# Performance work log

Hardware: AMD Instinct MI355X
Metric: run time of the kernel (lower is better)

Reference implementation:

```python
import jax, jax.numpy as jnp
import numpy as np

B, L_VLM, L_EXP = 4, 768, 64
L_TOT = L_VLM + L_EXP
D_VLM, D_EXP = 2048, 1024
H, DH = 8, 256
ROPE_BASE = 10000.0
SCALE = 1.0 / np.sqrt(DH).astype(np.float32)


def setup_inputs() -> dict:
    key = jax.random.key(0)
    ks = jax.random.split(key, 12)
    s = 0.02  # weight init scale
    return {
        "vlm_hidden": jax.random.normal(ks[0], (B, L_VLM, D_VLM), jnp.float32),
        "exp_hidden": jax.random.normal(ks[1], (B, L_EXP, D_EXP), jnp.float32),
        "attention_mask": jnp.zeros((B, 1, L_TOT, L_TOT), jnp.float32),  # additive mask
        "position_ids": jnp.broadcast_to(jnp.arange(L_TOT, dtype=jnp.int32)[None, :], (B, L_TOT)),
        "wq_v": jax.random.normal(ks[2], (D_VLM, H * DH), jnp.float32) * s,
        "wk_v": jax.random.normal(ks[3], (D_VLM, H * DH), jnp.float32) * s,
        "wv_v": jax.random.normal(ks[4], (D_VLM, H * DH), jnp.float32) * s,
        "wo_v": jax.random.normal(ks[5], (H * DH, D_VLM), jnp.float32) * s,
        "wq_e": jax.random.normal(ks[6], (D_EXP, H * DH), jnp.float32) * s,
        "wk_e": jax.random.normal(ks[7], (D_EXP, H * DH), jnp.float32) * s,
        "wv_e": jax.random.normal(ks[8], (D_EXP, H * DH), jnp.float32) * s,
        "wo_e": jax.random.normal(ks[9], (H * DH, D_EXP), jnp.float32) * s,
    }


def _proj(hs, w):
    # [B, L, D] @ [D, H*DH] -> [B, H, L, DH]
    b, l, _ = hs.shape
    return jnp.einsum('bld,de->ble', hs, w).reshape(b, l, H, DH).transpose(0, 2, 1, 3)


def _rope(x, cos, sin):
    # NeoX-style rotate-half (Gemma / vLLM RotaryEmbedding with rotary_dim == head_dim)
    d2 = x.shape[-1] // 2
    x1, x2 = x[..., :d2], x[..., d2:]
    return jnp.concatenate([x1 * cos - x2 * sin, x2 * cos + x1 * sin], axis=-1)


def reference(vlm_hidden, exp_hidden, attention_mask, position_ids,
              wq_v, wk_v, wv_v, wo_v, wq_e, wk_e, wv_e, wo_e):
    # 1) separate per-stream Q/K/V projections, 2) concat along sequence dim
    q = jnp.concatenate([_proj(vlm_hidden, wq_v), _proj(exp_hidden, wq_e)], axis=2)
    k = jnp.concatenate([_proj(vlm_hidden, wk_v), _proj(exp_hidden, wk_e)], axis=2)
    v = jnp.concatenate([_proj(vlm_hidden, wv_v), _proj(exp_hidden, wv_e)], axis=2)

    # 3) rotary positional embedding on the joint sequence
    inv_freq = 1.0 / (ROPE_BASE ** (jnp.arange(0, DH, 2, dtype=jnp.float32) / DH))  # [DH/2]
    freqs = position_ids.astype(jnp.float32)[:, :, None] * inv_freq                 # [B, L, DH/2]
    cos = jnp.cos(freqs)[:, None]  # [B, 1, L, DH/2]
    sin = jnp.sin(freqs)[:, None]
    q = _rope(q, cos, sin)
    k = _rope(k, cos, sin)

    # 4) masked attention over the joint sequence
    scores = jnp.einsum('bhqd,bhkd->bhqk', q, k) * SCALE + attention_mask
    probs = jax.nn.softmax(scores, axis=-1)
    out = jnp.einsum('bhqk,bhkd->bhqd', probs, v)              # [B, H, L, DH]
    out = out.transpose(0, 2, 1, 3).reshape(B, L_TOT, H * DH)  # [B, L, H*DH]

    # 5) split back and apply per-stream output projections
    vlm_out = jnp.einsum('ble,ed->bld', out[:, :L_VLM], wo_v)
    exp_out = jnp.einsum('ble,ed->bld', out[:, L_VLM:], wo_e)
    return vlm_out, exp_out
```

## Files before the change

### kernel.cpp

```cpp
#include <hip/hip_runtime.h>

typedef unsigned short u16;
using bf16x8 = __attribute__((ext_vector_type(8))) __bf16;
using f32x4  = __attribute__((ext_vector_type(4))) float;

__device__ __forceinline__ u16 f2bf(float f) {
  unsigned u = __builtin_bit_cast(unsigned, f);
  u += 0x7FFFu + ((u >> 16) & 1u);
  return (u16)(u >> 16);
}
__device__ __forceinline__ float bf2f(u16 s) {
  unsigned u = ((unsigned)s) << 16;
  return __builtin_bit_cast(float, u);
}
__device__ __forceinline__ void lds16(const void* g, void* l) {
  __builtin_amdgcn_global_load_lds(
      (const __attribute__((address_space(1))) void*)g,
      (__attribute__((address_space(3))) void*)l, 16, 0, 0);
}

__device__ __forceinline__ void gemm128(
    const u16* a0, const u16* a1, const u16* b0, const u16* b1,
    int ksteps, int t, u16* As, u16* Bs, f32x4 acc[4][4])
{
  const int lane = t & 63;
  u16* dA0 = As + t * 8;
  u16* dA1 = As + t * 8 + 2048;
  u16* dB0 = Bs + t * 8;
  u16* dB1 = Bs + t * 8 + 2048;

  const int wm = t >> 7;
  const int wn = (t >> 6) & 1;
  const int swz = (((lane >> 4) ^ (lane & 3)) * 8);
  const int fa = (wm * 64 + (lane & 15)) * 32 + swz;
  const int fb = (wn * 64 + (lane & 15)) * 32 + swz;

  for (int ks = 0; ks < ksteps; ++ks) {
    lds16(a0, dA0);
    lds16(a1, dA1);
    lds16(b0, dB0);
    lds16(b1, dB1);
    a0 += 32; a1 += 32; b0 += 32; b1 += 32;
    __syncthreads();
    bf16x8 af[4], bfr[4];
#pragma unroll
    for (int i = 0; i < 4; ++i) af[i]  = *(const bf16x8*)(As + fa + i * 512);
#pragma unroll
    for (int i = 0; i < 4; ++i) bfr[i] = *(const bf16x8*)(Bs + fb + i * 512);
#pragma unroll
    for (int mt = 0; mt < 4; ++mt)
#pragma unroll
      for (int nt = 0; nt < 4; ++nt)
        acc[mt][nt] = __builtin_amdgcn_mfma_f32_16x16x32_bf16(
            af[mt], bfr[nt], acc[mt][nt], 0, 0, 0);
    __syncthreads();
  }
}

struct PrepArgs {
  const float* tsrc[8]; u16* tdst[8]; int tK[8]; int tN[8];
  const float* csrc[2]; u16* cdst[2]; int cn4[2];
};

__global__ __launch_bounds__(256) void g_prep(PrepArgs a)
{
  __shared__ float T[32][33];
  const int z = blockIdx.z;
  if (z < 8) {
    const int Krows = a.tK[z], Ncols = a.tN[z];
    const int k0 = blockIdx.y * 32, n0 = blockIdx.x * 32;
    if (k0 >= Krows || n0 >= Ncols) return;
    const float* W = a.tsrc[z];
    u16* Wt = a.tdst[z];
    const int tx = threadIdx.x & 31, ty = threadIdx.x >> 5;
#pragma unroll
    for (int r = 0; r < 4; ++r)
      T[ty + r * 8][tx] = W[(size_t)(k0 + ty + r * 8) * Ncols + n0 + tx];
    __syncthreads();
#pragma unroll
    for (int r = 0; r < 4; ++r)
      Wt[(size_t)(n0 + ty + r * 8) * Krows + k0 + tx] = f2bf(T[tx][ty + r * 8]);
  } else {
    const int j = z - 8;
    const int n4 = a.cn4[j];
    const float* X = a.csrc[j];
    u16* Y = a.cdst[j];
    const int blk = blockIdx.y * gridDim.x + blockIdx.x;
    const int stride = gridDim.x * gridDim.y * 256;
    for (int i = blk * 256 + threadIdx.x; i < n4; i += stride) {
      float4 f = ((const float4*)X)[i];
      ushort4 u;
      u.x = f2bf(f.x); u.y = f2bf(f.y); u.z = f2bf(f.z); u.w = f2bf(f.w);
      ((ushort4*)Y)[i] = u;
    }
  }
}

__global__ __launch_bounds__(256) void g_proj_qkv(
    const u16* __restrict__ Xv, const u16* __restrict__ Xe,
    const u16* __restrict__ Wv_cat, const u16* __restrict__ We_cat,
    u16* __restrict__ Qb, u16* __restrict__ Kb, u16* __restrict__ Vt)
{
  __shared__ u16 As[4096], Bs[4096];
  const int z = blockIdx.z;
  const u16* X; const u16* Wt; int Kdim, rows_pb, l_off;
  if (z == 0) { X = Xv; Wt = Wv_cat; Kdim = 2048; rows_pb = 768; l_off = 0; }
  else {
    if (blockIdx.y >= 2) return;
    X = Xe; Wt = We_cat; Kdim = 1024; rows_pb = 64; l_off = 768;
  }
  const int t = threadIdx.x;
  const int m0 = blockIdx.y * 128, n0 = blockIdx.x * 128;
  const int r0 = t >> 2;
  const int cs = ((t & 3) ^ (r0 & 3)) * 8;
  const u16* a0 = X + (size_t)(m0 + r0) * Kdim + cs;
  const u16* a1 = X + (size_t)(m0 + r0 + 64) * Kdim + cs;
  const u16* b0 = Wt + (size_t)(n0 + r0) * Kdim + cs;
  const u16* b1 = Wt + (size_t)(n0 + r0 + 64) * Kdim + cs;

  f32x4 acc[4][4] = {};
  gemm128(a0, a1, b0, b1, Kdim >> 5, t, As, Bs, acc);

  const int lane = t & 63;
  const int rbase = m0 + (t >> 7) * 64 + ((lane >> 4) << 2);
  const int cbase = n0 + ((t >> 6) & 1) * 64 + (lane & 15);
  const int sect = n0 >> 11;

  if (sect < 2) {
    u16* Out = (sect == 0) ? Qb : Kb;
#pragma unroll
    for (int mt = 0; mt < 4; ++mt) {
#pragma unroll
      for (int r = 0; r < 4; ++r) {
        int m = rbase + mt * 16 + r;
        int b = m / rows_pb;
        int l = m - b * rows_pb + l_off;
#pragma unroll
        for (int nt = 0; nt < 4; ++nt) {
          int nloc = (cbase + nt * 16) & 2047;
          Out[(((size_t)(b * 8 + (nloc >> 8))) * 832 + l) * 256 + (nloc & 255)] =
              f2bf(acc[mt][nt][r]);
        }
      }
    }
  } else {
#pragma unroll
    for (int mt = 0; mt < 4; ++mt) {
      int mb = rbase + mt * 16;
      int b = mb / rows_pb;
      int l = mb - b * rows_pb + l_off;
#pragma unroll
      for (int nt = 0; nt < 4; ++nt) {
        int nloc = (cbase + nt * 16) & 2047;
        ushort4 p;
        p.x = f2bf(acc[mt][nt][0]); p.y = f2bf(acc[mt][nt][1]);
        p.z = f2bf(acc[mt][nt][2]); p.w = f2bf(acc[mt][nt][3]);
        *(ushort4*)&Vt[(((size_t)(b * 8 + (nloc >> 8))) * 256 + (nloc & 255)) * 832 + l] = p;
      }
    }
  }
}

__global__ __launch_bounds__(128) void g_rope(
    u16* __restrict__ Q, u16* __restrict__ Kx, const int* __restrict__ pos)
{
  const int blk = blockIdx.x;
  const int l = blk % 832, bh = blk / 832, b = bh >> 3;
  const int i = threadIdx.x;
  const float p = (float)pos[b * 832 + l];
  const float inv = exp2f(-(float)i * 0.103810252965229910f);
  const float ang = p * inv;
  const float c = cosf(ang), s = sinf(ang);
  const size_t base = ((size_t)bh * 832 + l) * 256;

  float x1 = bf2f(Q[base + i]), x2 = bf2f(Q[base + i + 128]);
  Q[base + i]       = f2bf((x1 * c - x2 * s) * 0.0625f);
  Q[base + i + 128] = f2bf((x2 * c + x1 * s) * 0.0625f);
  x1 = bf2f(Kx[base + i]); x2 = bf2f(Kx[base + i + 128]);
  Kx[base + i]       = f2bf(x1 * c - x2 * s);
  Kx[base + i + 128] = f2bf(x2 * c + x1 * s);
}

__global__ __launch_bounds__(256) void g_flash(
    const u16* __restrict__ Qb, const u16* __restrict__ Kb,
    const u16* __restrict__ Vt, const float* __restrict__ mask,
    u16* __restrict__ AO)
{
  __shared__ __align__(16) u16 Ks[8192];
  __shared__ __align__(16) u16 Vs[8192];
  __shared__ __align__(16) u16 Ps[2048];
  const int t = threadIdx.x;
  const int lane = t & 63, w = t >> 6, quad = lane >> 4;
  const int wb = w * 512;

  const int id = blockIdx.x;
  const int x = id & 7, k = id >> 3;
  const int bh = x + 8 * (k / 13);
  const int q0 = (k % 13) * 64;
  const int b = bh >> 3, h = bh & 7;

  const u16* Ksrc = Kb + (size_t)bh * 832 * 256;
  const u16* Vsrc = Vt + (size_t)bh * 256 * 832;
  const float* Mrow = mask + (size_t)b * 832 * 832;

  bf16x8 qf[8];
#pragma unroll
  for (int kf = 0; kf < 8; ++kf)
    qf[kf] = *(const bf16x8*)(
        Qb + ((size_t)bh * 832 + q0 + w * 16 + (lane & 15)) * 256 +
        kf * 32 + quad * 8);

  float mrun[4], lrun[4];
#pragma unroll
  for (int r = 0; r < 4; ++r) { mrun[r] = -3e38f; lrun[r] = 0.f; }
  f32x4 oa[16] = {};

  for (int kt = 0; kt < 26; ++kt) {
    __syncthreads();
#pragma unroll
    for (int p = 0; p < 4; ++p) {
      int c = p * 256 + t;
      int row = c >> 5, chk = c & 31;
      lds16(Ksrc + (size_t)(kt * 32 + row) * 256 + ((chk ^ (row & 7)) * 8),
            Ks + c * 8);
    }
#pragma unroll
    for (int p = 0; p < 4; ++p) {
      int c = p * 256 + t;
      int row = c >> 3;
      int lc = (c & 7) ^ (row & 7);
      int dh = 2 * row + (lc >> 2);
      lds16(Vsrc + (size_t)dh * 832 + kt * 32 + (lc & 3) * 8, Vs + c * 8);
    }
    __syncthreads();

    f32x4 sa[2] = {};
#pragma unroll
    for (int ks = 0; ks < 8; ++ks)
#pragma unroll
      for (int nt = 0; nt < 2; ++nt) {
        int krow = nt * 16 + (lane & 15);
        bf16x8 kb = *(const bf16x8*)(
            Ks + krow * 256 + (((ks * 4 + quad) ^ (krow & 7)) * 8));
        sa[nt] = __builtin_amdgcn_mfma_f32_16x16x32_bf16(qf[ks], kb, sa[nt], 0, 0, 0);
      }

    float alpha[4];
#pragma unroll
    for (int r = 0; r < 4; ++r) {
      int prow = quad * 4 + r;
      int q = q0 + w * 16 + prow;
      const float* mrp = Mrow + (size_t)q * 832 + kt * 32 + (lane & 15);
      float v0 = sa[0][r] + mrp[0];
      float v1 = sa[1][r] + mrp[16];
      float mx = fmaxf(v0, v1);
      mx = fmaxf(mx, __shfl_xor(mx, 1));
      mx = fmaxf(mx, __shfl_xor(mx, 2));
      mx = fmaxf(mx, __shfl_xor(mx, 4));
      mx = fmaxf(mx, __shfl_xor(mx, 8));
      float mn = fmaxf(mrun[r], mx);
      float al = __expf(mrun[r] - mn);
      float p0 = __expf(v0 - mn), p1 = __expf(v1 - mn);
      float rs = p0 + p1;
      rs += __shfl_xor(rs, 1);
      rs += __shfl_xor(rs, 2);
      rs += __shfl_xor(rs, 4);
      rs += __shfl_xor(rs, 8);
      lrun[r] = lrun[r] * al + rs;
      mrun[r] = mn;
      alpha[r] = al;
      int s0 = ((lane >> 3) & 1) ^ quad;
      int s1 = (2 | ((lane >> 3) & 1)) ^ quad;
      Ps[wb + prow * 32 + s0 * 8 + (lane & 7)] = f2bf(p0);
      Ps[wb + prow * 32 + s1 * 8 + (lane & 7)] = f2bf(p1);
    }

#pragma unroll
    for (int nt = 0; nt < 16; ++nt)
#pragma unroll
      for (int r = 0; r < 4; ++r) oa[nt][r] *= alpha[r];

    int prow2 = lane & 15;
    bf16x8 pa = *(const bf16x8*)(
        Ps + wb + prow2 * 32 + ((quad ^ ((prow2 >> 2) & 3)) * 8));
#pragma unroll
    for (int nt = 0; nt < 16; ++nt) {
      int dh = nt * 16 + (lane & 15);
      int row = dh >> 1;
      int lc = ((dh & 1) << 2) | quad;
      bf16x8 vb = *(const bf16x8*)(Vs + row * 64 + ((lc ^ (row & 7)) * 8));
      oa[nt] = __builtin_amdgcn_mfma_f32_16x16x32_bf16(pa, vb, oa[nt], 0, 0, 0);
    }
  }

  float linv[4];
#pragma unroll
  for (int r = 0; r < 4; ++r) linv[r] = 1.0f / lrun[r];
#pragma unroll
  for (int r = 0; r < 4; ++r) {
    size_t l = q0 + w * 16 + quad * 4 + r;
    u16* dst = AO + ((size_t)b * 832 + l) * 2048 + h * 256 + (lane & 15);
#pragma unroll
    for (int nt = 0; nt < 16; ++nt)
      dst[nt * 16] = f2bf(oa[nt][r] * linv[r]);
  }
}

__global__ __launch_bounds__(256) void g_oproj2(
    const u16* __restrict__ AO, const u16* __restrict__ Wov,
    const u16* __restrict__ Woe, float* __restrict__ out)
{
  __shared__ u16 As[4096], Bs[4096];
  const int z = blockIdx.z;
  const u16* Wt; float* C; int N, rows_pb, l_off;
  if (z == 0) { Wt = Wov; C = out; N = 2048; rows_pb = 768; l_off = 0; }
  else {
    if (blockIdx.y >= 2 || blockIdx.x >= 8) return;
    Wt = Woe; C = out + (size_t)4 * 768 * 2048; N = 1024; rows_pb = 64; l_off = 768;
  }
  const int t = threadIdx.x;
  const int m0 = blockIdx.y * 128, n0 = blockIdx.x * 128;
  const int r0 = t >> 2;
  const int cs = ((t & 3) ^ (r0 & 3)) * 8;
  int mr0 = m0 + r0, mr1 = m0 + r0 + 64;
  int ba = mr0 / rows_pb, bb = mr1 / rows_pb;
  const u16* a0 = AO + ((size_t)ba * 832 + (mr0 - ba * rows_pb) + l_off) * 2048 + cs;
  const u16* a1 = AO + ((size_t)bb * 832 + (mr1 - bb * rows_pb) + l_off) * 2048 + cs;
  const u16* b0 = Wt + (size_t)(n0 + r0) * 2048 + cs;
  const u16* b1 = Wt + (size_t)(n0 + r0 + 64) * 2048 + cs;

  f32x4 acc[4][4] = {};
  gemm128(a0, a1, b0, b1, 64, t, As, Bs, acc);

  const int lane = t & 63;
  const int rbase = m0 + (t >> 7) * 64 + ((lane >> 4) << 2);
  const int cbase = n0 + ((t >> 6) & 1) * 64 + (lane & 15);
#pragma unroll
  for (int mt = 0; mt < 4; ++mt)
#pragma unroll
    for (int r = 0; r < 4; ++r) {
      size_t m = rbase + mt * 16 + r;
#pragma unroll
      for (int nt = 0; nt < 4; ++nt)
        C[m * N + cbase + nt * 16] = acc[mt][nt][r];
    }
}

extern "C" void kernel_launch(void* const* d_in, const int* in_sizes, int n_in,
                              void* d_out, int out_size, void* d_ws, size_t ws_size,
                              hipStream_t stream)
{
  const float* vlm_h = (const float*)d_in[0];
  const float* exp_h = (const float*)d_in[1];
  const float* mask  = (const float*)d_in[2];
  const int*   pos   = (const int*)d_in[3];
  const float* wq_v  = (const float*)d_in[4];
  const float* wk_v  = (const float*)d_in[5];
  const float* wv_v  = (const float*)d_in[6];
  const float* wo_v  = (const float*)d_in[7];
  const float* wq_e  = (const float*)d_in[8];
  const float* wk_e  = (const float*)d_in[9];
  const float* wv_e  = (const float*)d_in[10];
  const float* wo_e  = (const float*)d_in[11];
  float* out = (float*)d_out;

  u16* U = (u16*)d_ws;
  u16* Xv   = U; U += (size_t)4 * 768 * 2048;
  u16* Xe   = U; U += (size_t)4 * 64 * 1024;
  u16* Wcv  = U; U += (size_t)6144 * 2048;
  u16* Wce  = U; U += (size_t)6144 * 1024;
  u16* Wov  = U; U += (size_t)2048 * 2048;
  u16* Woe  = U; U += (size_t)1024 * 2048;
  u16* Qb   = U; U += (size_t)32 * 832 * 256;
  u16* Kb   = U; U += (size_t)32 * 832 * 256;
  u16* Vt   = U; U += (size_t)32 * 256 * 832;
  u16* AO   = U; U += (size_t)4 * 832 * 2048;

  const dim3 blk(256);

  PrepArgs pa;
  pa.tsrc[0] = wq_v; pa.tdst[0] = Wcv;                        pa.tK[0] = 2048; pa.tN[0] = 2048;
  pa.tsrc[1] = wk_v; pa.tdst[1] = Wcv + (size_t)2048 * 2048;  pa.tK[1] = 2048; pa.tN[1] = 2048;
  pa.tsrc[2] = wv_v; pa.tdst[2] = Wcv + (size_t)4096 * 2048;  pa.tK[2] = 2048; pa.tN[2] = 2048;
  pa.tsrc[3] = wo_v; pa.tdst[3] = Wov;                        pa.tK[3] = 2048; pa.tN[3] = 2048;
  pa.tsrc[4] = wq_e; pa.tdst[4] = Wce;                        pa.tK[4] = 1024; pa.tN[4] = 2048;
  pa.tsrc[5] = wk_e; pa.tdst[5] = Wce + (size_t)2048 * 1024;  pa.tK[5] = 1024; pa.tN[5] = 2048;
  pa.tsrc[6] = wv_e; pa.tdst[6] = Wce + (size_t)4096 * 1024;  pa.tK[6] = 1024; pa.tN[6] = 2048;
  pa.tsrc[7] = wo_e; pa.tdst[7] = Woe;                        pa.tK[7] = 2048; pa.tN[7] = 1024;
  pa.csrc[0] = vlm_h; pa.cdst[0] = Xv; pa.cn4[0] = 1572864;
  pa.csrc[1] = exp_h; pa.cdst[1] = Xe; pa.cn4[1] = 65536;
  g_prep<<<dim3(64, 64, 10), blk, 0, stream>>>(pa);

  g_proj_qkv<<<dim3(48, 24, 2), blk, 0, stream>>>(Xv, Xe, Wcv, Wce, Qb, Kb, Vt);

  g_rope<<<dim3(32 * 832), dim3(128), 0, stream>>>(Qb, Kb, pos);

  g_flash<<<dim3(416), blk, 0, stream>>>(Qb, Kb, Vt, mask, AO);

  g_oproj2<<<dim3(16, 24, 2), blk, 0, stream>>>(AO, Wov, Woe, out);
}
```

Baseline: 456.3 us.

## Pipeline projection GEMMs with double-buffered LDS prefetch and phased MFMA scheduling

Replaces the single-stage GEMM core, which loaded one 32-wide K slice and synchronized twice per step, with a double-buffered 64-wide K pipeline. Global-to-LDS loads for upcoming tiles are issued in sub-phases, interleaved with MFMA groups, and paced with explicit vmcnt waits, barriers and setprio. The LDS swizzle changes to match the new fragment addressing. The goal is to hide global load latency behind matrix math in the QKV and output projections, at the cost of four times the LDS per block, which may lower occupancy, and fragile hand-tuned wait counts.

```diff
diff --git a/kernel.cpp b/kernel.cpp
--- a/kernel.cpp
+++ b/kernel.cpp
@@ -19,41 +19,110 @@
       (__attribute__((address_space(3))) void*)l, 16, 0, 0);
 }
 
-__device__ __forceinline__ void gemm128(
-    const u16* a0, const u16* a1, const u16* b0, const u16* b1,
-    int ksteps, int t, u16* As, u16* Bs, f32x4 acc[4][4])
+#define PH_SYNC() \
+  __builtin_amdgcn_s_barrier(); \
+  asm volatile("s_waitcnt lgkmcnt(0)" ::: "memory"); \
+  __builtin_amdgcn_sched_barrier(0);
+
+#define MFMA8(MA, MB) \
+  __builtin_amdgcn_s_setprio(1); \
+  acc[MA][0] = __builtin_amdgcn_mfma_f32_16x16x32_bf16(a0, b0, acc[MA][0], 0, 0, 0); \
+  acc[MB][0] = __builtin_amdgcn_mfma_f32_16x16x32_bf16(a1, b0, acc[MB][0], 0, 0, 0); \
+  acc[MA][1] = __builtin_amdgcn_mfma_f32_16x16x32_bf16(a0, b1, acc[MA][1], 0, 0, 0); \
+  acc[MB][1] = __builtin_amdgcn_mfma_f32_16x16x32_bf16(a1, b1, acc[MB][1], 0, 0, 0); \
+  acc[MA][2] = __builtin_amdgcn_mfma_f32_16x16x32_bf16(a0, b2, acc[MA][2], 0, 0, 0); \
+  acc[MB][2] = __builtin_amdgcn_mfma_f32_16x16x32_bf16(a1, b2, acc[MB][2], 0, 0, 0); \
+  acc[MA][3] = __builtin_amdgcn_mfma_f32_16x16x32_bf16(a0, b3, acc[MA][3], 0, 0, 0); \
+  acc[MB][3] = __builtin_amdgcn_mfma_f32_16x16x32_bf16(a1, b3, acc[MB][3], 0, 0, 0); \
+  __builtin_amdgcn_s_setprio(0);
+
+__device__ __forceinline__ void gemm_dp(
+    const u16* aR0, const u16* aR1, const u16* bR0, const u16* bR1,
+    int NT, int t, u16* As, u16* Bs, f32x4 acc[4][4])
 {
   const int lane = t & 63;
-  u16* dA0 = As + t * 8;
-  u16* dA1 = As + t * 8 + 2048;
-  u16* dB0 = Bs + t * 8;
-  u16* dB1 = Bs + t * 8 + 2048;
-
-  const int wm = t >> 7;
-  const int wn = (t >> 6) & 1;
-  const int swz = (((lane >> 4) ^ (lane & 3)) * 8);
-  const int fa = (wm * 64 + (lane & 15)) * 32 + swz;
-  const int fb = (wn * 64 + (lane & 15)) * 32 + swz;
-
-  for (int ks = 0; ks < ksteps; ++ks) {
-    lds16(a0, dA0);
-    lds16(a1, dA1);
-    lds16(b0, dB0);
-    lds16(b1, dB1);
-    a0 += 32; a1 += 32; b0 += 32; b1 += 32;
-    __syncthreads();
-    bf16x8 af[4], bfr[4];
-#pragma unroll
-    for (int i = 0; i < 4; ++i) af[i]  = *(const bf16x8*)(As + fa + i * 512);
-#pragma unroll
-    for (int i = 0; i < 4; ++i) bfr[i] = *(const bf16x8*)(Bs + fb + i * 512);
-#pragma unroll
-    for (int mt = 0; mt < 4; ++mt)
-#pragma unroll
-      for (int nt = 0; nt < 4; ++nt)
-        acc[mt][nt] = __builtin_amdgcn_mfma_f32_16x16x32_bf16(
-            af[mt], bfr[nt], acc[mt][nt], 0, 0, 0);
-    __syncthreads();
+  const int fr = lane & 15;
+  const int sA = ((lane >> 4) ^ ((fr >> 1) & 3)) << 3;
+  const int offA = (((t >> 7) & 1) * 64 + fr) * 32 + sA;
+  const int offB = (((t >> 6) & 1) * 64 + fr) * 32 + sA;
+
+  lds16(aR0,      As + t * 8);
+  lds16(aR1,      As + 2048 + t * 8);
+  lds16(bR0,      Bs + t * 8);
+  lds16(bR1,      Bs + 2048 + t * 8);
+  lds16(aR0 + 32, As + 4096 + t * 8);
+  lds16(aR1 + 32, As + 4096 + 2048 + t * 8);
+  lds16(bR0 + 32, Bs + 4096 + t * 8);
+  lds16(bR1 + 32, Bs + 4096 + 2048 + t * 8);
+  lds16(bR0 + 64, Bs + 8192 + t * 8);
+  lds16(bR1 + 64, Bs + 8192 + 2048 + t * 8);
+  lds16(aR0 + 64, As + 8192 + t * 8);
+  lds16(aR1 + 64, As + 8192 + 2048 + t * 8);
+  lds16(bR0 + 96, Bs + 8192 + 4096 + t * 8);
+  lds16(bR1 + 96, Bs + 8192 + 4096 + 2048 + t * 8);
+  asm volatile("s_waitcnt vmcnt(10)" ::: "memory");
+  __builtin_amdgcn_s_barrier();
+
+  for (int T = 0; T < NT; ++T) {
+    const int p = T & 1;
+    u16* Ab = As + p * 8192;
+    u16* Bb = Bs + p * 8192;
+    u16* An = As + (p ^ 1) * 8192;
+    const bool s1 = (T + 1 < NT), s2 = (T + 2 < NT);
+    const int k1 = (T + 1) * 64, k2 = (T + 2) * 64;
+    bf16x8 a0, a1, b0, b1, b2, b3;
+
+    a0 = *(const bf16x8*)(Ab + offA);
+    a1 = *(const bf16x8*)(Ab + offA + 512);
+    b0 = *(const bf16x8*)(Bb + offB);
+    b1 = *(const bf16x8*)(Bb + offB + 512);
+    b2 = *(const bf16x8*)(Bb + offB + 1024);
+    b3 = *(const bf16x8*)(Bb + offB + 1536);
+    if (s1) {
+      lds16(aR0 + k1 + 32, An + 4096 + t * 8);
+      lds16(aR1 + k1 + 32, An + 4096 + 2048 + t * 8);
+    }
+    PH_SYNC();
+    MFMA8(0, 1);
+    __builtin_amdgcn_s_barrier();
+
+    a0 = *(const bf16x8*)(Ab + offA + 1024);
+    a1 = *(const bf16x8*)(Ab + offA + 1536);
+    if (s2) {
+      lds16(bR0 + k2, Bb + t * 8);
+      lds16(bR1 + k2, Bb + 2048 + t * 8);
+    }
+    PH_SYNC();
+    MFMA8(2, 3);
+    if (s2) asm volatile("s_waitcnt vmcnt(10)" ::: "memory");
+    else    asm volatile("s_waitcnt vmcnt(0)"  ::: "memory");
+    __builtin_amdgcn_s_barrier();
+
+    a0 = *(const bf16x8*)(Ab + offA + 4096);
+    a1 = *(const bf16x8*)(Ab + offA + 4096 + 512);
+    b0 = *(const bf16x8*)(Bb + offB + 4096);
+    b1 = *(const bf16x8*)(Bb + offB + 4096 + 512);
+    b2 = *(const bf16x8*)(Bb + offB + 4096 + 1024);
+    b3 = *(const bf16x8*)(Bb + offB + 4096 + 1536);
+    if (s2) {
+      lds16(aR0 + k2, Ab + t * 8);
+      lds16(aR1 + k2, Ab + 2048 + t * 8);
+    }
+    PH_SYNC();
+    MFMA8(0, 1);
+    __builtin_amdgcn_s_barrier();
+
+    a0 = *(const bf16x8*)(Ab + offA + 4096 + 1024);
+    a1 = *(const bf16x8*)(Ab + offA + 4096 + 1536);
+    if (s2) {
+      lds16(bR0 + k2 + 32, Bb + 4096 + t * 8);
+      lds16(bR1 + k2 + 32, Bb + 4096 + 2048 + t * 8);
+    }
+    PH_SYNC();
+    MFMA8(2, 3);
+    if (s2) asm volatile("s_waitcnt vmcnt(10)" ::: "memory");
+    else    asm volatile("s_waitcnt vmcnt(0)"  ::: "memory");
+    __builtin_amdgcn_s_barrier();
   }
 }
 
@@ -101,7 +170,7 @@
     const u16* __restrict__ Wv_cat, const u16* __restrict__ We_cat,
     u16* __restrict__ Qb, u16* __restrict__ Kb, u16* __restrict__ Vt)
 {
-  __shared__ u16 As[4096], Bs[4096];
+  __shared__ __align__(16) u16 As[16384], Bs[16384];
   const int z = blockIdx.z;
   const u16* X; const u16* Wt; int Kdim, rows_pb, l_off;
   if (z == 0) { X = Xv; Wt = Wv_cat; Kdim = 2048; rows_pb = 768; l_off = 0; }
@@ -112,14 +181,14 @@
   const int t = threadIdx.x;
   const int m0 = blockIdx.y * 128, n0 = blockIdx.x * 128;
   const int r0 = t >> 2;
-  const int cs = ((t & 3) ^ (r0 & 3)) * 8;
-  const u16* a0 = X + (size_t)(m0 + r0) * Kdim + cs;
-  const u16* a1 = X + (size_t)(m0 + r0 + 64) * Kdim + cs;
-  const u16* b0 = Wt + (size_t)(n0 + r0) * Kdim + cs;
-  const u16* b1 = Wt + (size_t)(n0 + r0 + 64) * Kdim + cs;
+  const int sw = ((t & 3) ^ ((t >> 3) & 3)) * 8;
+  const u16* a0 = X + (size_t)(m0 + r0) * Kdim + sw;
+  const u16* a1 = X + (size_t)(m0 + r0 + 64) * Kdim + sw;
+  const u16* b0 = Wt + (size_t)(n0 + r0) * Kdim + sw;
+  const u16* b1 = Wt + (size_t)(n0 + r0 + 64) * Kdim + sw;
 
   f32x4 acc[4][4] = {};
-  gemm128(a0, a1, b0, b1, Kdim >> 5, t, As, Bs, acc);
+  gemm_dp(a0, a1, b0, b1, Kdim >> 6, t, As, Bs, acc);
 
   const int lane = t & 63;
   const int rbase = m0 + (t >> 7) * 64 + ((lane >> 4) << 2);
@@ -310,7 +379,7 @@
     const u16* __restrict__ AO, const u16* __restrict__ Wov,
     const u16* __restrict__ Woe, float* __restrict__ out)
 {
-  __shared__ u16 As[4096], Bs[4096];
+  __shared__ __align__(16) u16 As[16384], Bs[16384];
   const int z = blockIdx.z;
   const u16* Wt; float* C; int N, rows_pb, l_off;
   if (z == 0) { Wt = Wov; C = out; N = 2048; rows_pb = 768; l_off = 0; }
@@ -321,16 +390,16 @@
   const int t = threadIdx.x;
   const int m0 = blockIdx.y * 128, n0 = blockIdx.x * 128;
   const int r0 = t >> 2;
-  const int cs = ((t & 3) ^ (r0 & 3)) * 8;
+  const int sw = ((t & 3) ^ ((t >> 3) & 3)) * 8;
   int mr0 = m0 + r0, mr1 = m0 + r0 + 64;
   int ba = mr0 / rows_pb, bb = mr1 / rows_pb;
-  const u16* a0 = AO + ((size_t)ba * 832 + (mr0 - ba * rows_pb) + l_off) * 2048 + cs;
-  const u16* a1 = AO + ((size_t)bb * 832 + (mr1 - bb * rows_pb) + l_off) * 2048 + cs;
-  const u16* b0 = Wt + (size_t)(n0 + r0) * 2048 + cs;
-  const u16* b1 = Wt + (size_t)(n0 + r0 + 64) * 2048 + cs;
+  const u16* a0 = AO + ((size_t)ba * 832 + (mr0 - ba * rows_pb) + l_off) * 2048 + sw;
+  const u16* a1 = AO + ((size_t)bb * 832 + (mr1 - bb * rows_pb) + l_off) * 2048 + sw;
+  const u16* b0 = Wt + (size_t)(n0 + r0) * 2048 + sw;
+  const u16* b1 = Wt + (size_t)(n0 + r0 + 64) * 2048 + sw;
 
   f32x4 acc[4][4] = {};
-  gemm128(a0, a1, b0, b1, 64, t, As, Bs, acc);
+  gemm_dp(a0, a1, b0, b1, 32, t, As, Bs, acc);
 
   const int lane = t & 63;
   const int rbase = m0 + (t >> 7) * 64 + ((lane >> 4) << 2);
```

New measurement: 445.6 us. -2.4%, faster.

## Triple-buffer GEMM LDS loads with 256x128 tiles and 512-thread blocks

Applied to the files above, without the earlier changes.

Replaces the synchronous single-buffer 128x128 GEMM loop with a three-stage LDS ring that prefetches two K-steps ahead using direct global-to-LDS loads, explicit waitcnt, barriers and raised MFMA priority. QKV and output projection blocks grow to 512 threads covering 256x128 tiles, and the expert-stream blocks are folded into the same grid instead of a separate z slice. This is meant to hide global load latency behind MFMA work and halve the B-tile traffic per output. In exchange it uses more LDS per block and may lower occupancy, and the hand-placed waitcnt and barrier sequence is fragile.

```diff
diff --git a/kernel.cpp b/kernel.cpp
--- a/kernel.cpp
+++ b/kernel.cpp
@@ -19,41 +19,66 @@
       (__attribute__((address_space(3))) void*)l, 16, 0, 0);
 }
 
-__device__ __forceinline__ void gemm128(
-    const u16* a0, const u16* a1, const u16* b0, const u16* b1,
-    int ksteps, int t, u16* As, u16* Bs, f32x4 acc[4][4])
-{
-  const int lane = t & 63;
-  u16* dA0 = As + t * 8;
-  u16* dA1 = As + t * 8 + 2048;
-  u16* dB0 = Bs + t * 8;
-  u16* dB1 = Bs + t * 8 + 2048;
-
-  const int wm = t >> 7;
-  const int wn = (t >> 6) & 1;
-  const int swz = (((lane >> 4) ^ (lane & 3)) * 8);
-  const int fa = (wm * 64 + (lane & 15)) * 32 + swz;
-  const int fb = (wn * 64 + (lane & 15)) * 32 + swz;
-
-  for (int ks = 0; ks < ksteps; ++ks) {
-    lds16(a0, dA0);
-    lds16(a1, dA1);
-    lds16(b0, dB0);
-    lds16(b1, dB1);
-    a0 += 32; a1 += 32; b0 += 32; b1 += 32;
-    __syncthreads();
-    bf16x8 af[4], bfr[4];
-#pragma unroll
-    for (int i = 0; i < 4; ++i) af[i]  = *(const bf16x8*)(As + fa + i * 512);
-#pragma unroll
-    for (int i = 0; i < 4; ++i) bfr[i] = *(const bf16x8*)(Bs + fb + i * 512);
-#pragma unroll
-    for (int mt = 0; mt < 4; ++mt)
-#pragma unroll
-      for (int nt = 0; nt < 4; ++nt)
-        acc[mt][nt] = __builtin_amdgcn_mfma_f32_16x16x32_bf16(
-            af[mt], bfr[nt], acc[mt][nt], 0, 0, 0);
-    __syncthreads();
+#define MM(A, B, C) __builtin_amdgcn_mfma_f32_16x16x32_bf16(A, B, C, 0, 0, 0)
+
+#define MFMA16() \
+  __builtin_amdgcn_s_setprio(1); \
+  acc[0][0]=MM(a0,b0,acc[0][0]); acc[0][1]=MM(a0,b1,acc[0][1]); \
+  acc[0][2]=MM(a0,b2,acc[0][2]); acc[0][3]=MM(a0,b3,acc[0][3]); \
+  acc[1][0]=MM(a1,b0,acc[1][0]); acc[1][1]=MM(a1,b1,acc[1][1]); \
+  acc[1][2]=MM(a1,b2,acc[1][2]); acc[1][3]=MM(a1,b3,acc[1][3]); \
+  acc[2][0]=MM(a2,b0,acc[2][0]); acc[2][1]=MM(a2,b1,acc[2][1]); \
+  acc[2][2]=MM(a2,b2,acc[2][2]); acc[2][3]=MM(a2,b3,acc[2][3]); \
+  acc[3][0]=MM(a3,b0,acc[3][0]); acc[3][1]=MM(a3,b1,acc[3][1]); \
+  acc[3][2]=MM(a3,b2,acc[3][2]); acc[3][3]=MM(a3,b3,acc[3][3]); \
+  __builtin_amdgcn_s_setprio(0);
+
+__device__ __forceinline__ void gemm_rg(
+    const u16* aS0, const u16* aS1, const u16* bS0,
+    int NT, int t, u16* As, u16* Bs, f32x4 (&acc)[4][4])
+{
+  const int lane = t & 63, fr = lane & 15, q4 = lane >> 4;
+  const int w = t >> 6, wm = w >> 1, wn = w & 1;
+  const int sxy = (q4 ^ ((fr >> 1) & 3)) * 8;
+  const int aoff = (wm * 64 + fr) * 32 + sxy;
+  const int boff = (wn * 64 + fr) * 32 + sxy;
+
+  lds16(aS0,      As + t * 8);
+  lds16(aS1,      As + 4096 + t * 8);
+  lds16(bS0,      Bs + t * 8);
+  lds16(aS0 + 32, As + 8192 + t * 8);
+  lds16(aS1 + 32, As + 8192 + 4096 + t * 8);
+  lds16(bS0 + 32, Bs + 4096 + t * 8);
+  asm volatile("s_waitcnt vmcnt(3)" ::: "memory");
+  __builtin_amdgcn_s_barrier();
+
+  for (int T = 0; T < NT; ++T) {
+    const int q = T % 3;
+    const u16* Ab = As + q * 8192;
+    const u16* Bb = Bs + q * 4096;
+    bf16x8 a0 = *(const bf16x8*)(Ab + aoff);
+    bf16x8 a1 = *(const bf16x8*)(Ab + aoff + 512);
+    bf16x8 a2 = *(const bf16x8*)(Ab + aoff + 1024);
+    bf16x8 a3 = *(const bf16x8*)(Ab + aoff + 1536);
+    bf16x8 b0 = *(const bf16x8*)(Bb + boff);
+    bf16x8 b1 = *(const bf16x8*)(Bb + boff + 512);
+    bf16x8 b2 = *(const bf16x8*)(Bb + boff + 1024);
+    bf16x8 b3 = *(const bf16x8*)(Bb + boff + 1536);
+    const bool s2 = (T + 2 < NT);
+    if (s2) {
+      const int q2 = (T + 2) % 3;
+      const int k2 = (T + 2) * 32;
+      lds16(aS0 + k2, As + q2 * 8192 + t * 8);
+      lds16(aS1 + k2, As + q2 * 8192 + 4096 + t * 8);
+      lds16(bS0 + k2, Bs + q2 * 4096 + t * 8);
+    }
+    __builtin_amdgcn_s_barrier();
+    asm volatile("s_waitcnt lgkmcnt(0)" ::: "memory");
+    __builtin_amdgcn_sched_barrier(0);
+    MFMA16();
+    if (s2) asm volatile("s_waitcnt vmcnt(3)" ::: "memory");
+    else    asm volatile("s_waitcnt vmcnt(0)" ::: "memory");
+    __builtin_amdgcn_s_barrier();
   }
 }
 
@@ -96,34 +121,31 @@
   }
 }
 
-__global__ __launch_bounds__(256) void g_proj_qkv(
+__global__ __launch_bounds__(512, 4) void g_proj_qkv(
     const u16* __restrict__ Xv, const u16* __restrict__ Xe,
     const u16* __restrict__ Wv_cat, const u16* __restrict__ We_cat,
     u16* __restrict__ Qb, u16* __restrict__ Kb, u16* __restrict__ Vt)
 {
-  __shared__ u16 As[4096], Bs[4096];
-  const int z = blockIdx.z;
-  const u16* X; const u16* Wt; int Kdim, rows_pb, l_off;
-  if (z == 0) { X = Xv; Wt = Wv_cat; Kdim = 2048; rows_pb = 768; l_off = 0; }
-  else {
-    if (blockIdx.y >= 2) return;
-    X = Xe; Wt = We_cat; Kdim = 1024; rows_pb = 64; l_off = 768;
-  }
+  __shared__ __align__(16) u16 As[24576], Bs[12288];
+  const int y = blockIdx.y;
+  const u16* X; const u16* Wt; int Kdim, rows_pb, l_off, m0;
+  if (y < 12) { X = Xv; Wt = Wv_cat; Kdim = 2048; rows_pb = 768; l_off = 0; m0 = y * 256; }
+  else        { X = Xe; Wt = We_cat; Kdim = 1024; rows_pb = 64;  l_off = 768; m0 = 0; }
   const int t = threadIdx.x;
-  const int m0 = blockIdx.y * 128, n0 = blockIdx.x * 128;
-  const int r0 = t >> 2;
-  const int cs = ((t & 3) ^ (r0 & 3)) * 8;
-  const u16* a0 = X + (size_t)(m0 + r0) * Kdim + cs;
-  const u16* a1 = X + (size_t)(m0 + r0 + 64) * Kdim + cs;
-  const u16* b0 = Wt + (size_t)(n0 + r0) * Kdim + cs;
-  const u16* b1 = Wt + (size_t)(n0 + r0 + 64) * Kdim + cs;
+  const int n0 = blockIdx.x * 128;
+  const int r = t >> 2;
+  const int swk = ((t & 3) ^ ((t >> 3) & 3)) * 8;
+  const u16* aS0 = X + (size_t)(m0 + r) * Kdim + swk;
+  const u16* aS1 = X + (size_t)(m0 + r + 128) * Kdim + swk;
+  const u16* bS0 = Wt + (size_t)(n0 + r) * Kdim + swk;
 
   f32x4 acc[4][4] = {};
-  gemm128(a0, a1, b0, b1, Kdim >> 5, t, As, Bs, acc);
-
-  const int lane = t & 63;
-  const int rbase = m0 + (t >> 7) * 64 + ((lane >> 4) << 2);
-  const int cbase = n0 + ((t >> 6) & 1) * 64 + (lane & 15);
+  gemm_rg(aS0, aS1, bS0, Kdim >> 5, t, As, Bs, acc);
+
+  const int lane = t & 63, fr = lane & 15, q4 = lane >> 4;
+  const int w = t >> 6, wm = w >> 1, wn = w & 1;
+  const int rbase = m0 + wm * 64 + q4 * 4;
+  const int cbase = n0 + wn * 64 + fr;
   const int sect = n0 >> 11;
 
   if (sect < 2) {
@@ -131,15 +153,15 @@
 #pragma unroll
     for (int mt = 0; mt < 4; ++mt) {
 #pragma unroll
-      for (int r = 0; r < 4; ++r) {
-        int m = rbase + mt * 16 + r;
+      for (int rr = 0; rr < 4; ++rr) {
+        int m = rbase + mt * 16 + rr;
         int b = m / rows_pb;
         int l = m - b * rows_pb + l_off;
 #pragma unroll
         for (int nt = 0; nt < 4; ++nt) {
           int nloc = (cbase + nt * 16) & 2047;
           Out[(((size_t)(b * 8 + (nloc >> 8))) * 832 + l) * 256 + (nloc & 255)] =
-              f2bf(acc[mt][nt][r]);
+              f2bf(acc[mt][nt][rr]);
         }
       }
     }
@@ -306,43 +328,43 @@
   }
 }
 
-__global__ __launch_bounds__(256) void g_oproj2(
+__global__ __launch_bounds__(512, 4) void g_oproj2(
     const u16* __restrict__ AO, const u16* __restrict__ Wov,
     const u16* __restrict__ Woe, float* __restrict__ out)
 {
-  __shared__ u16 As[4096], Bs[4096];
-  const int z = blockIdx.z;
-  const u16* Wt; float* C; int N, rows_pb, l_off;
-  if (z == 0) { Wt = Wov; C = out; N = 2048; rows_pb = 768; l_off = 0; }
+  __shared__ __align__(16) u16 As[24576], Bs[12288];
+  const int y = blockIdx.y;
+  const u16* Wt; float* C; int N, rows_pb, l_off, m0;
+  if (y < 12) { Wt = Wov; C = out; N = 2048; rows_pb = 768; l_off = 0; m0 = y * 256; }
   else {
-    if (blockIdx.y >= 2 || blockIdx.x >= 8) return;
-    Wt = Woe; C = out + (size_t)4 * 768 * 2048; N = 1024; rows_pb = 64; l_off = 768;
+    if (blockIdx.x >= 8) return;
+    Wt = Woe; C = out + (size_t)4 * 768 * 2048; N = 1024; rows_pb = 64; l_off = 768; m0 = 0;
   }
   const int t = threadIdx.x;
-  const int m0 = blockIdx.y * 128, n0 = blockIdx.x * 128;
-  const int r0 = t >> 2;
-  const int cs = ((t & 3) ^ (r0 & 3)) * 8;
-  int mr0 = m0 + r0, mr1 = m0 + r0 + 64;
+  const int n0 = blockIdx.x * 128;
+  const int r = t >> 2;
+  const int swk = ((t & 3) ^ ((t >> 3) & 3)) * 8;
+  int mr0 = m0 + r, mr1 = m0 + r + 128;
   int ba = mr0 / rows_pb, bb = mr1 / rows_pb;
-  const u16* a0 = AO + ((size_t)ba * 832 + (mr0 - ba * rows_pb) + l_off) * 2048 + cs;
-  const u16* a1 = AO + ((size_t)bb * 832 + (mr1 - bb * rows_pb) + l_off) * 2048 + cs;
-  const u16* b0 = Wt + (size_t)(n0 + r0) * 2048 + cs;
-  const u16* b1 = Wt + (size_t)(n0 + r0 + 64) * 2048 + cs;
+  const u16* aS0 = AO + ((size_t)ba * 832 + (mr0 - ba * rows_pb) + l_off) * 2048 + swk;
+  const u16* aS1 = AO + ((size_t)bb * 832 + (mr1 - bb * rows_pb) + l_off) * 2048 + swk;
+  const u16* bS0 = Wt + (size_t)(n0 + r) * 2048 + swk;
 
   f32x4 acc[4][4] = {};
-  gemm128(a0, a1, b0, b1, 64, t, As, Bs, acc);
-
-  const int lane = t & 63;
-  const int rbase = m0 + (t >> 7) * 64 + ((lane >> 4) << 2);
-  const int cbase = n0 + ((t >> 6) & 1) * 64 + (lane & 15);
+  gemm_rg(aS0, aS1, bS0, 64, t, As, Bs, acc);
+
+  const int lane = t & 63, fr = lane & 15, q4 = lane >> 4;
+  const int w = t >> 6, wm = w >> 1, wn = w & 1;
+  const int rbase = m0 + wm * 64 + q4 * 4;
+  const int cbase = n0 + wn * 64 + fr;
 #pragma unroll
   for (int mt = 0; mt < 4; ++mt)
 #pragma unroll
-    for (int r = 0; r < 4; ++r) {
-      size_t m = rbase + mt * 16 + r;
+    for (int rr = 0; rr < 4; ++rr) {
+      size_t m = rbase + mt * 16 + rr;
 #pragma unroll
       for (int nt = 0; nt < 4; ++nt)
-        C[m * N + cbase + nt * 16] = acc[mt][nt][r];
+        C[m * N + cbase + nt * 16] = acc[mt][nt][rr];
     }
 }
 
@@ -391,11 +413,11 @@
   pa.csrc[1] = exp_h; pa.cdst[1] = Xe; pa.cn4[1] = 65536;
   g_prep<<<dim3(64, 64, 10), blk, 0, stream>>>(pa);
 
-  g_proj_qkv<<<dim3(48, 24, 2), blk, 0, stream>>>(Xv, Xe, Wcv, Wce, Qb, Kb, Vt);
+  g_proj_qkv<<<dim3(48, 13, 1), dim3(512), 0, stream>>>(Xv, Xe, Wcv, Wce, Qb, Kb, Vt);
 
   g_rope<<<dim3(32 * 832), dim3(128), 0, stream>>>(Qb, Kb, pos);
 
   g_flash<<<dim3(416), blk, 0, stream>>>(Qb, Kb, Vt, mask, AO);
 
-  g_oproj2<<<dim3(16, 24, 2), blk, 0, stream>>>(AO, Wov, Woe, out);
-}
+  g_oproj2<<<dim3(16, 13, 1), dim3(512), 0, stream>>>(AO, Wov, Woe, out);
+}
```

Result: faster. 416.1 us (-8.8%).
